# Optimization experiments

Measured on AMD Instinct MI355X. Metric: run time of the kernel, lower is better.

The kernel has to match this reference:

```python
import jax, jax.numpy as jnp
import numpy as np

NUM_E = 100000
NUM_R = 500
HIDDEN = 64
BATCH = 32
GAMMA = 12.0
EPSILON = 2.0
EMB_RANGE = (GAMMA + EPSILON) / HIDDEN  # 0.21875
PI = 3.141592653589793


def setup_inputs() -> dict:
    key = jax.random.key(0)
    k1, k2, k3 = jax.random.split(key, 3)
    facts = jax.random.randint(k1, (BATCH, 3), 0, 1000, dtype=jnp.int64)  # col0<num_e, col1<2*num_r
    entity_embedding = jax.random.uniform(
        k2, (NUM_E, 2 * HIDDEN), dtype=jnp.float32, minval=-EMB_RANGE, maxval=EMB_RANGE)
    relation_embedding = jax.random.uniform(
        k3, (NUM_R * 2, HIDDEN), dtype=jnp.float32, minval=-EMB_RANGE, maxval=EMB_RANGE)
    return {"facts": facts, "entity_embedding": entity_embedding,
            "relation_embedding": relation_embedding}


def reference(facts, entity_embedding, relation_embedding):
    # Gather head/relation embeddings for the batch
    head = entity_embedding[facts[:, 0]]          # [B, 2D]
    relation = relation_embedding[facts[:, 1]]    # [B, D]

    re_head, im_head = jnp.split(head, 2, axis=1)           # [B, D] each
    re_tail, im_tail = jnp.split(entity_embedding, 2, axis=1)  # [E, D] each

    phase = relation / (EMB_RANGE / PI)
    re_rel = jnp.cos(phase)
    im_rel = jnp.sin(phase)

    # Complex rotation of head by relation: [B, D]
    re_rot = re_head * re_rel - im_head * im_rel
    im_rot = re_head * im_rel + im_head * re_rel

    # Broadcast difference against all entities: [B, E, D]
    re_diff = re_rot[:, None, :] - re_tail[None, :, :]
    im_diff = im_rot[:, None, :] - im_tail[None, :, :]

    # Per-component complex modulus, summed over dim -> [B, E]
    dist = jnp.sqrt(re_diff * re_diff + im_diff * im_diff).sum(axis=2)
    return GAMMA - dist
```

## Files before the change

### kernel.cpp

```cpp
#include <hip/hip_runtime.h>
#include <math.h>

#define NUM_E   100000
#define HIDDEN  64
#define BATCH   32
#define GAMMA_F 12.0f
#define EMB_RANGE_F 0.21875f
#define INV_TWO_EMB (1.0f / (2.0f * EMB_RANGE_F))

typedef float v4f __attribute__((ext_vector_type(4)));
typedef float v2f __attribute__((ext_vector_type(2)));

static __device__ __forceinline__ v2f pk_sub(v2f a, v2f b) {
    v2f d;
    asm("v_pk_add_f32 %0, %1, %2 neg_lo:[0,1] neg_hi:[0,1]"
        : "=v"(d) : "v"(a), "v"(b));
    return d;
}
static __device__ __forceinline__ v2f pk_mul(v2f a, v2f b) {
    v2f d;
    asm("v_pk_mul_f32 %0, %1, %2" : "=v"(d) : "v"(a), "v"(b));
    return d;
}
static __device__ __forceinline__ v2f pk_fma(v2f a, v2f b, v2f c) {
    v2f d;
    asm("v_pk_fma_f32 %0, %1, %2, %3" : "=v"(d) : "v"(a), "v"(b), "v"(c));
    return d;
}
static __device__ __forceinline__ float sq2(v2f dx, v2f dy) {
    v2f sq = pk_fma(dy, dy, pk_mul(dx, dx));
    return __builtin_amdgcn_sqrtf(sq.x) + __builtin_amdgcn_sqrtf(sq.y);
}
static __device__ __forceinline__ v2f lo2(v4f v) { return __builtin_shufflevector(v, v, 0, 1); }
static __device__ __forceinline__ v2f hi2(v4f v) { return __builtin_shufflevector(v, v, 2, 3); }

template <int CTRL>
static __device__ __forceinline__ float dpp_xor_add(float x) {
    int y = __builtin_amdgcn_update_dpp(0, __float_as_int(x), CTRL, 0xF, 0xF, true);
    return x + __int_as_float(y);
}

__global__ void rotate_phase_kernel(const int* __restrict__ facts,
                                    const float* __restrict__ ent,
                                    const float* __restrict__ rel,
                                    float* __restrict__ rot) {
    int p = blockIdx.x * blockDim.x + threadIdx.x;
    if (p >= BATCH * HIDDEN) return;
    int b = p >> 6;
    int d = p & 63;
    int f0 = facts[b * 3 + 0];
    int f1 = facts[b * 3 + 1];
    float hre = ent[(size_t)f0 * 128 + d];
    float him = ent[(size_t)f0 * 128 + 64 + d];
    float r   = rel[(size_t)f1 * 64 + d];
    float rev = r * INV_TWO_EMB;
    float s = __builtin_amdgcn_sinf(rev);
    float c = __builtin_amdgcn_cosf(rev);
    rot[p]                  = hre * c - him * s;
    rot[BATCH * HIDDEN + p] = hre * s + him * c;
}

__global__ __launch_bounds__(256, 4) void rotate_dist_kernel(
        const float* __restrict__ ent,
        const float* __restrict__ rot,
        float* __restrict__ out) {
    __shared__ float s_ent[4096];
    __shared__ float s_scr[4][136];

    const int t    = threadIdx.x;
    const int lane = t & 63;
    const int wv   = t >> 6;
    const int bg   = lane >> 3;
    const int dg   = lane & 7;
    const int e0   = blockIdx.x * 32 + wv * 8;

    v2f RR[4][4], RI[4][4];
#pragma unroll
    for (int kb = 0; kb < 4; ++kb) {
        const v4f* pr = (const v4f*)(rot + (bg * 4 + kb) * 64 + dg * 8);
        const v4f* pi = (const v4f*)(rot + 2048 + (bg * 4 + kb) * 64 + dg * 8);
        v4f a = pr[0], b = pr[1], c = pi[0], d = pi[1];
        RR[kb][0] = lo2(a); RR[kb][1] = hi2(a); RR[kb][2] = lo2(b); RR[kb][3] = hi2(b);
        RI[kb][0] = lo2(c); RI[kb][1] = hi2(c); RI[kb][2] = lo2(d); RI[kb][3] = hi2(d);
    }

    float* lds = s_ent + wv * 1024;
    {
        const v4f* g4 = (const v4f*)(ent + (size_t)e0 * 128);
        v4f* s4 = (v4f*)lds;
#pragma unroll
        for (int k = 0; k < 4; ++k) s4[k * 64 + lane] = g4[k * 64 + lane];
    }

    float* scr = s_scr[wv];

#pragma unroll 1
    for (int grp = 0; grp < 2; ++grp) {
        float p[4][4];

#pragma unroll
        for (int i = 0; i < 4; ++i) {
            const float* base = lds + (grp * 4 + i) * 128 + dg * 8;
            v4f er0 = *(const v4f*)(base);
            v4f er1 = *(const v4f*)(base + 4);
            v4f ei0 = *(const v4f*)(base + 64);
            v4f ei1 = *(const v4f*)(base + 68);
            v2f e2[4] = { lo2(er0), hi2(er0), lo2(er1), hi2(er1) };
            v2f i2[4] = { lo2(ei0), hi2(ei0), lo2(ei1), hi2(ei1) };
#pragma unroll
            for (int kb = 0; kb < 4; ++kb) {
                float s0 = sq2(pk_sub(RR[kb][0], e2[0]), pk_sub(RI[kb][0], i2[0]));
                float s1 = sq2(pk_sub(RR[kb][1], e2[1]), pk_sub(RI[kb][1], i2[1]));
                float s2 = sq2(pk_sub(RR[kb][2], e2[2]), pk_sub(RI[kb][2], i2[2]));
                float s3 = sq2(pk_sub(RR[kb][3], e2[3]), pk_sub(RI[kb][3], i2[3]));
                p[i][kb] = (s0 + s1) + (s2 + s3);
            }
        }

#pragma unroll
        for (int i = 0; i < 4; ++i)
#pragma unroll
            for (int kb = 0; kb < 4; ++kb) {
                float v = p[i][kb];
                v = dpp_xor_add<0xB1>(v);
                v = dpp_xor_add<0x4E>(v);
                v += __shfl_xor(v, 4, 64);
                p[i][kb] = GAMMA_F - v;
            }

        if (dg < 4) {
#pragma unroll
            for (int i = 0; i < 4; ++i) {
                float val = (dg == 0) ? p[i][0] : (dg == 1) ? p[i][1]
                          : (dg == 2) ? p[i][2] : p[i][3];
                scr[i * 33 + bg * 4 + dg] = val;
            }
        }
#pragma unroll
        for (int j = 0; j < 2; ++j) {
            const int b  = (lane >> 2) + 16 * j;
            const int el = lane & 3;
            float v = scr[el * 33 + b];
            out[(size_t)b * NUM_E + e0 + grp * 4 + el] = v;
        }
    }
}

extern "C" void kernel_launch(void* const* d_in, const int* in_sizes, int n_in,
                              void* d_out, int out_size, void* d_ws, size_t ws_size,
                              hipStream_t stream) {
    const int*   facts = (const int*)d_in[0];
    const float* ent   = (const float*)d_in[1];
    const float* rel   = (const float*)d_in[2];
    float*       out   = (float*)d_out;
    float*       rot   = (float*)d_ws;

    rotate_phase_kernel<<<dim3((BATCH * HIDDEN + 255) / 256), dim3(256), 0, stream>>>(
        facts, ent, rel, rot);

    rotate_dist_kernel<<<dim3(NUM_E / 32), dim3(256), 0, stream>>>(
        ent, rot, out);
}
```

Before: 118.4 us.

## Fuse phase rotation into distance kernel and loop over five entity tiles per block

Drops the separate rotation kernel. Each thread now recomputes its rotated head values, via sin/cos and a gather, directly in the distance kernel. To spread that recompute cost, the grid shrinks from 3125 to 625 blocks, each processing five 32-entity tiles in a loop. The goal is to remove a launch and the global round trip through workspace, at the cost of redundant transcendental work per block and fewer blocks to spread across CUs.

```diff
diff --git a/kernel.cpp b/kernel.cpp
--- a/kernel.cpp
+++ b/kernel.cpp
@@ -40,108 +40,115 @@
     return x + __int_as_float(y);
 }
 
-__global__ void rotate_phase_kernel(const int* __restrict__ facts,
-                                    const float* __restrict__ ent,
-                                    const float* __restrict__ rel,
-                                    float* __restrict__ rot) {
-    int p = blockIdx.x * blockDim.x + threadIdx.x;
-    if (p >= BATCH * HIDDEN) return;
-    int b = p >> 6;
-    int d = p & 63;
-    int f0 = facts[b * 3 + 0];
-    int f1 = facts[b * 3 + 1];
-    float hre = ent[(size_t)f0 * 128 + d];
-    float him = ent[(size_t)f0 * 128 + 64 + d];
-    float r   = rel[(size_t)f1 * 64 + d];
-    float rev = r * INV_TWO_EMB;
-    float s = __builtin_amdgcn_sinf(rev);
-    float c = __builtin_amdgcn_cosf(rev);
-    rot[p]                  = hre * c - him * s;
-    rot[BATCH * HIDDEN + p] = hre * s + him * c;
-}
-
-__global__ __launch_bounds__(256, 4) void rotate_dist_kernel(
+__global__ __launch_bounds__(256, 4) void rotate_fused_kernel(
+        const int* __restrict__ facts,
         const float* __restrict__ ent,
-        const float* __restrict__ rot,
+        const float* __restrict__ rel,
         float* __restrict__ out) {
     __shared__ float s_ent[4096];
-    __shared__ float s_scr[4][136];
+    __shared__ float s_scr[4][4 * 40];
 
     const int t    = threadIdx.x;
     const int lane = t & 63;
     const int wv   = t >> 6;
     const int bg   = lane >> 3;
     const int dg   = lane & 7;
-    const int e0   = blockIdx.x * 32 + wv * 8;
 
     v2f RR[4][4], RI[4][4];
 #pragma unroll
     for (int kb = 0; kb < 4; ++kb) {
-        const v4f* pr = (const v4f*)(rot + (bg * 4 + kb) * 64 + dg * 8);
-        const v4f* pi = (const v4f*)(rot + 2048 + (bg * 4 + kb) * 64 + dg * 8);
-        v4f a = pr[0], b = pr[1], c = pi[0], d = pi[1];
-        RR[kb][0] = lo2(a); RR[kb][1] = hi2(a); RR[kb][2] = lo2(b); RR[kb][3] = hi2(b);
-        RI[kb][0] = lo2(c); RI[kb][1] = hi2(c); RI[kb][2] = lo2(d); RI[kb][3] = hi2(d);
+        const int b  = bg * 4 + kb;
+        const int f0 = facts[b * 3 + 0];
+        const int f1 = facts[b * 3 + 1];
+        const float* hb = ent + (size_t)f0 * 128 + dg * 8;
+        const float* rb = rel + (size_t)f1 * 64 + dg * 8;
+        v4f hr0 = *(const v4f*)(hb);
+        v4f hr1 = *(const v4f*)(hb + 4);
+        v4f hm0 = *(const v4f*)(hb + 64);
+        v4f hm1 = *(const v4f*)(hb + 68);
+        v4f rl0 = *(const v4f*)(rb);
+        v4f rl1 = *(const v4f*)(rb + 4);
+        float hre[8] = {hr0.x, hr0.y, hr0.z, hr0.w, hr1.x, hr1.y, hr1.z, hr1.w};
+        float him[8] = {hm0.x, hm0.y, hm0.z, hm0.w, hm1.x, hm1.y, hm1.z, hm1.w};
+        float rlv[8] = {rl0.x, rl0.y, rl0.z, rl0.w, rl1.x, rl1.y, rl1.z, rl1.w};
+        float Rr[8], Ri[8];
+#pragma unroll
+        for (int d = 0; d < 8; ++d) {
+            float rev = rlv[d] * INV_TWO_EMB;
+            float s = __builtin_amdgcn_sinf(rev);
+            float c = __builtin_amdgcn_cosf(rev);
+            Rr[d] = hre[d] * c - him[d] * s;
+            Ri[d] = hre[d] * s + him[d] * c;
+        }
+        RR[kb][0] = (v2f){Rr[0], Rr[1]}; RR[kb][1] = (v2f){Rr[2], Rr[3]};
+        RR[kb][2] = (v2f){Rr[4], Rr[5]}; RR[kb][3] = (v2f){Rr[6], Rr[7]};
+        RI[kb][0] = (v2f){Ri[0], Ri[1]}; RI[kb][1] = (v2f){Ri[2], Ri[3]};
+        RI[kb][2] = (v2f){Ri[4], Ri[5]}; RI[kb][3] = (v2f){Ri[6], Ri[7]};
     }
 
     float* lds = s_ent + wv * 1024;
-    {
-        const v4f* g4 = (const v4f*)(ent + (size_t)e0 * 128);
-        v4f* s4 = (v4f*)lds;
-#pragma unroll
-        for (int k = 0; k < 4; ++k) s4[k * 64 + lane] = g4[k * 64 + lane];
-    }
-
     float* scr = s_scr[wv];
 
 #pragma unroll 1
-    for (int grp = 0; grp < 2; ++grp) {
-        float p[4][4];
+    for (int tile = 0; tile < 5; ++tile) {
+        const int e0 = blockIdx.x * 160 + tile * 32 + wv * 8;
+
+        {
+            const v4f* g4 = (const v4f*)(ent + (size_t)e0 * 128);
+            v4f* s4 = (v4f*)lds;
+#pragma unroll
+            for (int k = 0; k < 4; ++k) s4[k * 64 + lane] = g4[k * 64 + lane];
+        }
+
+#pragma unroll 1
+        for (int grp = 0; grp < 2; ++grp) {
+            float p[4][4];
 
 #pragma unroll
-        for (int i = 0; i < 4; ++i) {
-            const float* base = lds + (grp * 4 + i) * 128 + dg * 8;
-            v4f er0 = *(const v4f*)(base);
-            v4f er1 = *(const v4f*)(base + 4);
-            v4f ei0 = *(const v4f*)(base + 64);
-            v4f ei1 = *(const v4f*)(base + 68);
-            v2f e2[4] = { lo2(er0), hi2(er0), lo2(er1), hi2(er1) };
-            v2f i2[4] = { lo2(ei0), hi2(ei0), lo2(ei1), hi2(ei1) };
+            for (int i = 0; i < 4; ++i) {
+                const float* base = lds + (grp * 4 + i) * 128 + dg * 8;
+                v4f er0 = *(const v4f*)(base);
+                v4f er1 = *(const v4f*)(base + 4);
+                v4f ei0 = *(const v4f*)(base + 64);
+                v4f ei1 = *(const v4f*)(base + 68);
+                v2f e2[4] = { lo2(er0), hi2(er0), lo2(er1), hi2(er1) };
+                v2f i2[4] = { lo2(ei0), hi2(ei0), lo2(ei1), hi2(ei1) };
 #pragma unroll
-            for (int kb = 0; kb < 4; ++kb) {
-                float s0 = sq2(pk_sub(RR[kb][0], e2[0]), pk_sub(RI[kb][0], i2[0]));
-                float s1 = sq2(pk_sub(RR[kb][1], e2[1]), pk_sub(RI[kb][1], i2[1]));
-                float s2 = sq2(pk_sub(RR[kb][2], e2[2]), pk_sub(RI[kb][2], i2[2]));
-                float s3 = sq2(pk_sub(RR[kb][3], e2[3]), pk_sub(RI[kb][3], i2[3]));
-                p[i][kb] = (s0 + s1) + (s2 + s3);
+                for (int kb = 0; kb < 4; ++kb) {
+                    float s0 = sq2(pk_sub(RR[kb][0], e2[0]), pk_sub(RI[kb][0], i2[0]));
+                    float s1 = sq2(pk_sub(RR[kb][1], e2[1]), pk_sub(RI[kb][1], i2[1]));
+                    float s2 = sq2(pk_sub(RR[kb][2], e2[2]), pk_sub(RI[kb][2], i2[2]));
+                    float s3 = sq2(pk_sub(RR[kb][3], e2[3]), pk_sub(RI[kb][3], i2[3]));
+                    p[i][kb] = (s0 + s1) + (s2 + s3);
+                }
             }
-        }
 
 #pragma unroll
-        for (int i = 0; i < 4; ++i)
+            for (int i = 0; i < 4; ++i)
 #pragma unroll
-            for (int kb = 0; kb < 4; ++kb) {
-                float v = p[i][kb];
-                v = dpp_xor_add<0xB1>(v);
-                v = dpp_xor_add<0x4E>(v);
-                v += __shfl_xor(v, 4, 64);
-                p[i][kb] = GAMMA_F - v;
+                for (int kb = 0; kb < 4; ++kb) {
+                    float v = p[i][kb];
+                    v = dpp_xor_add<0xB1>(v);
+                    v = dpp_xor_add<0x4E>(v);
+                    v += __shfl_xor(v, 4, 64);
+                    p[i][kb] = GAMMA_F - v;
+                }
+
+            if (dg < 4) {
+#pragma unroll
+                for (int i = 0; i < 4; ++i) {
+                    float val = (dg == 0) ? p[i][0] : (dg == 1) ? p[i][1]
+                              : (dg == 2) ? p[i][2] : p[i][3];
+                    scr[i * 40 + bg * 4 + dg] = val;
+                }
             }
-
-        if (dg < 4) {
 #pragma unroll
-            for (int i = 0; i < 4; ++i) {
-                float val = (dg == 0) ? p[i][0] : (dg == 1) ? p[i][1]
-                          : (dg == 2) ? p[i][2] : p[i][3];
-                scr[i * 33 + bg * 4 + dg] = val;
+            for (int j = 0; j < 2; ++j) {
+                const int b  = (lane >> 2) + 16 * j;
+                const int el = lane & 3;
+                float v = scr[el * 40 + b];
+                out[(size_t)b * NUM_E + e0 + grp * 4 + el] = v;
             }
-        }
-#pragma unroll
-        for (int j = 0; j < 2; ++j) {
-            const int b  = (lane >> 2) + 16 * j;
-            const int el = lane & 3;
-            float v = scr[el * 33 + b];
-            out[(size_t)b * NUM_E + e0 + grp * 4 + el] = v;
         }
     }
 }
@@ -153,11 +160,7 @@
     const float* ent   = (const float*)d_in[1];
     const float* rel   = (const float*)d_in[2];
     float*       out   = (float*)d_out;
-    float*       rot   = (float*)d_ws;
 
-    rotate_phase_kernel<<<dim3((BATCH * HIDDEN + 255) / 256), dim3(256), 0, stream>>>(
-        facts, ent, rel, rot);
-
-    rotate_dist_kernel<<<dim3(NUM_E / 32), dim3(256), 0, stream>>>(
-        ent, rot, out);
+    rotate_fused_kernel<<<dim3(625), dim3(256), 0, stream>>>(
+        facts, ent, rel, out);
 }
```

Result: slower. 128.6 us (+8.6%).
